# Performance work log

Hardware: AMD Instinct MI355X
Metric: run time of the kernel (lower is better)

Reference implementation:

```python
import jax, jax.numpy as jnp
import numpy as np

D_MODEL = 64  # per-head dim used in the scale sqrt(d_model*2)
B, H, S, D = 4, 16, 2048, 64


def setup_inputs() -> dict:
    key = jax.random.key(0)
    kq, kk, kv, kd, ke, km = jax.random.split(key, 6)
    return {
        "Q": jax.random.normal(kq, (B, H, S, D), dtype=jnp.float32),
        "K": jax.random.normal(kk, (B, H, S, D), dtype=jnp.float32),
        "V": jax.random.normal(kv, (B, H, S, D), dtype=jnp.float32),
        "distance_matrix": jax.random.uniform(kd, (B, S, S), dtype=jnp.float32),
        "energy_matrix": jax.random.uniform(ke, (B, S, S), dtype=jnp.float32),
        "mask": jax.random.randint(km, (B, 1, S, S), 0, 2, dtype=jnp.int32),
    }


def reference(Q, K, V, distance_matrix, energy_matrix, mask):
    # distance_matrix and energy_matrix are unused by the original forward.
    scale = 1.0 / np.sqrt(D_MODEL * 2).astype(np.float32)
    scores = jnp.einsum("bhqd,bhkd->bhqk", Q, K) * scale  # [B,H,S,S]
    scores = jnp.where(mask == 0, jnp.float32(-1e9), scores)
    attn = jax.nn.softmax(scores, axis=-1)
    context = jnp.einsum("bhqk,bhkd->bhqd", attn, V)  # [B,H,S,D]
    return context
```

## Files before the change

### kernel.cpp

```cpp
#include <hip/hip_runtime.h>
#include <stdint.h>

#define DEVINL __device__ __forceinline__

typedef float f32x4 __attribute__((ext_vector_type(4)));
typedef float f32x2 __attribute__((ext_vector_type(2)));
typedef short s16x8 __attribute__((ext_vector_type(8)));
typedef short s16x4 __attribute__((ext_vector_type(4)));
typedef unsigned int u32x4 __attribute__((ext_vector_type(4)));

constexpr int Bb = 4, Hh = 16, Ss = 2048, Dd = 64;
constexpr float SCALE = 0.088388347648318447f;
constexpr float QSC = 0.088388347648318447f * 1.4426950408889634f;

DEVINL short f2bf(float x) {
  union { float f; unsigned u; } c; c.f = x;
  unsigned r = (c.u + 0x7fffu + ((c.u >> 16) & 1u)) >> 16;
  return (short)r;
}

DEVINL unsigned pkbf(float a, float b) {
  unsigned r;
  asm("v_cvt_pk_bf16_f32 %0, %1, %2" : "=v"(r) : "v"(a), "v"(b));
  return r;
}

DEVINL void gload_lds16(const short* g, short* l) {
  __builtin_amdgcn_global_load_lds(
      (const __attribute__((address_space(1))) void*)g,
      (__attribute__((address_space(3))) void*)l, 16, 0, 0);
}

__global__ void mask_to_bits(const int* __restrict__ mask,
                             unsigned long long* __restrict__ bits, int n) {
  int gid = blockIdx.x * blockDim.x + threadIdx.x;
  int stride = gridDim.x * blockDim.x;
  for (int i = gid; i < n; i += stride) {
    unsigned long long bal = __ballot(mask[i] != 0);
    if ((i & 63) == 0) bits[i >> 6] = bal;
  }
}

__global__ void kvconv(const float* __restrict__ K, const float* __restrict__ V,
                       short* __restrict__ Kimg, short* __restrict__ Vimg) {
  const int x = blockIdx.x;
  const int sel = x & 1;
  const int t = (x >> 1) & 31;
  const int bh = x >> 6;
  const int tid = threadIdx.x;
  if (sel == 0) {
    const float* Kp = K + ((size_t)bh * Ss + t * 64) * Dd;
    short* img = Kimg + ((size_t)bh * 32 + t) * 4096;
#pragma unroll
    for (int it = 0; it < 4; ++it) {
      int idx = tid + it * 256;
      int kv = idx >> 4, c = idx & 15;
      const float* kr = Kp + (size_t)kv * Dd;
      s16x4 sv;
      sv[0] = f2bf(kr[c]);
      sv[1] = f2bf(kr[c + 16]);
      sv[2] = f2bf(kr[c + 32]);
      sv[3] = f2bf(kr[c + 48]);
      *(s16x4*)(img + kv * 64 + ((4 * c) ^ ((kv & 7) << 3))) = sv;
    }
  } else {
    const float* Vp = V + ((size_t)bh * Ss + t * 64) * Dd;
    short* img = Vimg + ((size_t)bh * 32 + t) * 4096;
    const int d = tid & 63, c4 = tid >> 6;
#pragma unroll
    for (int it = 0; it < 4; ++it) {
      int c = c4 * 4 + it;
      s16x4 sv;
      sv[0] = f2bf(Vp[(size_t)(c) * Dd + d]);
      sv[1] = f2bf(Vp[(size_t)(c + 16) * Dd + d]);
      sv[2] = f2bf(Vp[(size_t)(c + 32) * Dd + d]);
      sv[3] = f2bf(Vp[(size_t)(c + 48) * Dd + d]);
      *(s16x4*)(img + d * 64 + ((4 * c) ^ ((d & 7) << 3))) = sv;
    }
  }
}

__launch_bounds__(256, 4)
__global__ void attn2(const float* __restrict__ Q,
                      const unsigned long long* __restrict__ mbits,
                      const short* __restrict__ Kimg,
                      const short* __restrict__ Vimg,
                      float* __restrict__ Out) {
  __shared__ short lds[16384];

  const int tid = threadIdx.x;
  const int lane = tid & 63;
  const int w = tid >> 6;
  const int l15 = lane & 15;
  const int lq = lane >> 4;

  const int bid = blockIdx.x;
  const int h = bid & 15;
  const int qt = (bid >> 4) & 15;
  const int b = bid >> 8;
  const int bh = b * Hh + h;

  const float* Qp = Q + (size_t)bh * Ss * Dd;
  float* Op = Out + (size_t)bh * Ss * Dd;
  const short* Kt = Kimg + (size_t)bh * 32 * 4096;
  const short* Vt = Vimg + (size_t)bh * 32 * 4096;
  const int qbW = qt * 128 + w * 32;

  s16x8 qf[2][2];
#pragma unroll
  for (int qs = 0; qs < 2; ++qs) {
    const float* qrow = Qp + (size_t)(qbW + qs * 16 + l15) * Dd;
#pragma unroll
    for (int dh = 0; dh < 2; ++dh) {
      s16x8 f;
#pragma unroll
      for (int g = 0; g < 4; ++g) {
        f32x2 v = *(const f32x2*)(qrow + 16 * g + 4 * lq + 2 * dh);
        f[g] = f2bf(v[0] * QSC);
        f[g + 4] = f2bf(v[1] * QSC);
      }
      qf[qs][dh] = f;
    }
  }

  f32x4 oacc[2][4];
  float lpart[2] = {0.f, 0.f};
#pragma unroll
  for (int qs = 0; qs < 2; ++qs)
#pragma unroll
    for (int ds = 0; ds < 4; ++ds) oacc[qs][ds] = f32x4{0.f, 0.f, 0.f, 0.f};

  int off[4][2];
#pragma unroll
  for (int sub = 0; sub < 4; ++sub) {
    int row = sub * 16 + l15;
    int sw = (row & 7) << 3;
    off[sub][0] = row * 64 + ((16 * lq) ^ sw);
    off[sub][1] = row * 64 + ((16 * lq + 8) ^ sw);
  }

  auto stage = [&](int buf, int t) {
    short* Lb = lds + buf * 8192;
    const short* gk = Kt + t * 4096 + w * 512 + lane * 8;
    const short* gv = Vt + t * 4096 + w * 512 + lane * 8;
    gload_lds16(gk, Lb + w * 512);
    gload_lds16(gk + 2048, Lb + 2048 + w * 512);
    gload_lds16(gv, Lb + 4096 + w * 512);
    gload_lds16(gv + 2048, Lb + 6144 + w * 512);
  };

  stage(0, 0);

  for (int t = 0; t < 32; ++t) {
    const int cur = t & 1;
    __syncthreads();
    if (t < 31) stage(cur ^ 1, t + 1);

    const short* kb = lds + cur * 8192;
    const short* vb = kb + 4096;

    f32x4 sc[2][4];
#pragma unroll
    for (int sub = 0; sub < 4; ++sub) {
      s16x8 k0 = *(const s16x8*)(kb + off[sub][0]);
      s16x8 k1 = *(const s16x8*)(kb + off[sub][1]);
#pragma unroll
      for (int qs = 0; qs < 2; ++qs) {
        f32x4 a = f32x4{0.f, 0.f, 0.f, 0.f};
        a = __builtin_amdgcn_mfma_f32_16x16x32_bf16(k0, qf[qs][0], a, 0, 0, 0);
        a = __builtin_amdgcn_mfma_f32_16x16x32_bf16(k1, qf[qs][1], a, 0, 0, 0);
        sc[qs][sub] = a;
      }
    }

    s16x8 pf[2][2];
#pragma unroll
    for (int qs = 0; qs < 2; ++qs) {
      const int q = qbW + qs * 16 + l15;
      const unsigned long long mw = mbits[(size_t)(b * Ss + q) * 32 + t];
      const unsigned mlo = (unsigned)(mw >> (4 * lq));
      const unsigned mhi = (unsigned)(mw >> (32 + 4 * lq));
      const unsigned nibs[4] = {mlo & 15u, (mlo >> 16) & 15u, mhi & 15u, (mhi >> 16) & 15u};
      float ps = 0.f;
#pragma unroll
      for (int sub = 0; sub < 4; ++sub) {
        f32x4 s = sc[qs][sub];
        const unsigned nib = nibs[sub];
#pragma unroll
        for (int r = 0; r < 4; ++r) {
          float p = __builtin_amdgcn_exp2f(s[r]);
          p = ((nib >> r) & 1u) ? p : 0.f;
          s[r] = p;
          ps += p;
        }
        sc[qs][sub] = s;
      }
      lpart[qs] += ps;
#pragma unroll
      for (int kvh = 0; kvh < 2; ++kvh) {
        u32x4 wv;
        wv[0] = pkbf(sc[qs][0][2 * kvh], sc[qs][1][2 * kvh]);
        wv[1] = pkbf(sc[qs][2][2 * kvh], sc[qs][3][2 * kvh]);
        wv[2] = pkbf(sc[qs][0][2 * kvh + 1], sc[qs][1][2 * kvh + 1]);
        wv[3] = pkbf(sc[qs][2][2 * kvh + 1], sc[qs][3][2 * kvh + 1]);
        pf[qs][kvh] = __builtin_bit_cast(s16x8, wv);
      }
    }

#pragma unroll
    for (int ds = 0; ds < 4; ++ds) {
      s16x8 v0 = *(const s16x8*)(vb + off[ds][0]);
      s16x8 v1 = *(const s16x8*)(vb + off[ds][1]);
#pragma unroll
      for (int qs = 0; qs < 2; ++qs) {
        f32x4 a = oacc[qs][ds];
        a = __builtin_amdgcn_mfma_f32_16x16x32_bf16(v0, pf[qs][0], a, 0, 0, 0);
        a = __builtin_amdgcn_mfma_f32_16x16x32_bf16(v1, pf[qs][1], a, 0, 0, 0);
        oacc[qs][ds] = a;
      }
    }
  }

#pragma unroll
  for (int qs = 0; qs < 2; ++qs) {
    float l = lpart[qs];
    l += __shfl_xor(l, 16);
    l += __shfl_xor(l, 32);
    float inv = 1.f / l;
    float* orow = Op + (size_t)(qbW + qs * 16 + l15) * Dd;
#pragma unroll
    for (int ds = 0; ds < 4; ++ds) {
      f32x4 v = oacc[qs][ds];
      v *= inv;
      *(f32x4*)(orow + ds * 16 + 4 * lq) = v;
    }
  }
}

template<bool USEBITS>
__launch_bounds__(256, 2)
__global__ void attn_fwd(const float* __restrict__ Q, const float* __restrict__ K,
                         const float* __restrict__ V, const int* __restrict__ mask,
                         const unsigned long long* __restrict__ mbits,
                         float* __restrict__ Out) {
  __shared__ short Ks[64 * 64];
  __shared__ short Vs[64 * 64];

  const int tid = threadIdx.x;
  const int lane = tid & 63;
  const int w = tid >> 6;
  const int l15 = lane & 15;
  const int lq = lane >> 4;

  const int bid = blockIdx.x;
  const int h = bid & 15;
  const int qt = (bid >> 4) & 7;
  const int b = bid >> 7;

  const int bh = b * Hh + h;
  const float* Qp = Q + (size_t)bh * Ss * Dd;
  const float* Kp = K + (size_t)bh * Ss * Dd;
  const float* Vp = V + (size_t)bh * Ss * Dd;
  float* Op = Out + (size_t)bh * Ss * Dd;

  const int qbW = qt * 256 + w * 64;

  s16x8 qf[4][2];
#pragma unroll
  for (int qs = 0; qs < 4; ++qs) {
    const float* qrow = Qp + (size_t)(qbW + qs * 16 + l15) * Dd;
#pragma unroll
    for (int dh = 0; dh < 2; ++dh) {
      s16x8 f;
#pragma unroll
      for (int g = 0; g < 4; ++g) {
        f32x2 v = *(const f32x2*)(qrow + 16 * g + 4 * lq + 2 * dh);
        f[g] = f2bf(v[0]);
        f[g + 4] = f2bf(v[1]);
      }
      qf[qs][dh] = f;
    }
  }

  f32x4 oacc[4][4];
  float mrun[4], lrun[4];
#pragma unroll
  for (int qs = 0; qs < 4; ++qs) {
    mrun[qs] = -1e30f;
    lrun[qs] = 0.f;
#pragma unroll
    for (int ds = 0; ds < 4; ++ds) oacc[qs][ds] = f32x4{0.f, 0.f, 0.f, 0.f};
  }

  for (int kv0 = 0; kv0 < Ss; kv0 += 64) {
    __syncthreads();
#pragma unroll
    for (int p = 0; p < 4; ++p) {
      int f = tid + p * 256;
      int kv = f >> 4;
      int c = f & 15;
      const float* krow = Kp + (size_t)(kv0 + kv) * Dd;
      s16x4 sv;
      sv[0] = f2bf(krow[c]);
      sv[1] = f2bf(krow[c + 16]);
      sv[2] = f2bf(krow[c + 32]);
      sv[3] = f2bf(krow[c + 48]);
      *(s16x4*)(Ks + kv * 64 + ((4 * c) ^ ((kv & 7) << 3))) = sv;
    }
#pragma unroll
    for (int p = 0; p < 4; ++p) {
      int f = tid + p * 256;
      int kv = f >> 4;
      int c = f & 15;
      f32x4 v = *(const f32x4*)(Vp + (size_t)(kv0 + kv) * Dd + 4 * c);
      int pv = (kv & 15) * 4 + (kv >> 4);
#pragma unroll
      for (int i = 0; i < 4; ++i) {
        int d = 4 * c + i;
        Vs[d * 64 + (pv ^ ((d & 7) << 3))] = f2bf(v[i]);
      }
    }
    __syncthreads();

    s16x8 kf[4][2];
#pragma unroll
    for (int sub = 0; sub < 4; ++sub) {
      int row = sub * 16 + l15;
      const short* base = Ks + row * 64;
      int sw = (row & 7) << 3;
      kf[sub][0] = *(const s16x8*)(base + ((16 * lq + 0) ^ sw));
      kf[sub][1] = *(const s16x8*)(base + ((16 * lq + 8) ^ sw));
    }
    s16x8 vf[4][2];
#pragma unroll
    for (int ds = 0; ds < 4; ++ds) {
      int row = ds * 16 + l15;
      const short* base = Vs + row * 64;
      int sw = (row & 7) << 3;
      vf[ds][0] = *(const s16x8*)(base + ((16 * lq + 0) ^ sw));
      vf[ds][1] = *(const s16x8*)(base + ((16 * lq + 8) ^ sw));
    }

    const int kvw = kv0 >> 6;
#pragma unroll
    for (int qs = 0; qs < 4; ++qs) {
      f32x4 sc[4];
#pragma unroll
      for (int sub = 0; sub < 4; ++sub) {
        f32x4 a = f32x4{0.f, 0.f, 0.f, 0.f};
        a = __builtin_amdgcn_mfma_f32_16x16x32_bf16(kf[sub][0], qf[qs][0], a, 0, 0, 0);
        a = __builtin_amdgcn_mfma_f32_16x16x32_bf16(kf[sub][1], qf[qs][1], a, 0, 0, 0);
        sc[sub] = a;
      }

      const int q = qbW + qs * 16 + l15;
      unsigned long long mw = 0;
      if constexpr (USEBITS) mw = mbits[(size_t)(b * Ss + q) * 32 + kvw];

      float tm = -3e38f;
#pragma unroll
      for (int sub = 0; sub < 4; ++sub) {
        f32x4 s = sc[sub];
        if constexpr (USEBITS) {
          unsigned nib = (unsigned)((mw >> (16 * sub + 4 * lq)) & 0xFULL);
#pragma unroll
          for (int r = 0; r < 4; ++r) {
            float sv = s[r] * SCALE;
            sv = ((nib >> r) & 1u) ? sv : -1e9f;
            s[r] = sv;
            tm = fmaxf(tm, sv);
          }
        } else {
          const int* mrow = mask + ((size_t)b * Ss + q) * Ss + kv0 + 16 * sub + 4 * lq;
          int4 mi = *(const int4*)mrow;
          int mv[4] = {mi.x, mi.y, mi.z, mi.w};
#pragma unroll
          for (int r = 0; r < 4; ++r) {
            float sv = s[r] * SCALE;
            sv = mv[r] ? sv : -1e9f;
            s[r] = sv;
            tm = fmaxf(tm, sv);
          }
        }
        sc[sub] = s;
      }
      tm = fmaxf(tm, __shfl_xor(tm, 16));
      tm = fmaxf(tm, __shfl_xor(tm, 32));
      float mnew = fmaxf(mrun[qs], tm);
      float corr = __expf(mrun[qs] - mnew);
      mrun[qs] = mnew;

      float ps = 0.f;
#pragma unroll
      for (int sub = 0; sub < 4; ++sub) {
        f32x4 s = sc[sub];
#pragma unroll
        for (int r = 0; r < 4; ++r) {
          float p = __expf(s[r] - mnew);
          s[r] = p;
          ps += p;
        }
        sc[sub] = s;
      }
      ps += __shfl_xor(ps, 16);
      ps += __shfl_xor(ps, 32);
      lrun[qs] = lrun[qs] * corr + ps;
#pragma unroll
      for (int ds = 0; ds < 4; ++ds) oacc[qs][ds] *= corr;

      s16x8 pf[2];
#pragma unroll
      for (int kvh = 0; kvh < 2; ++kvh) {
        s16x8 f;
#pragma unroll
        for (int j = 0; j < 8; ++j) f[j] = f2bf(sc[j & 3][2 * kvh + (j >> 2)]);
        pf[kvh] = f;
      }
#pragma unroll
      for (int ds = 0; ds < 4; ++ds) {
        f32x4 a = oacc[qs][ds];
        a = __builtin_amdgcn_mfma_f32_16x16x32_bf16(vf[ds][0], pf[0], a, 0, 0, 0);
        a = __builtin_amdgcn_mfma_f32_16x16x32_bf16(vf[ds][1], pf[1], a, 0, 0, 0);
        oacc[qs][ds] = a;
      }
    }
  }

#pragma unroll
  for (int qs = 0; qs < 4; ++qs) {
    float inv = 1.f / lrun[qs];
    float* orow = Op + (size_t)(qbW + qs * 16 + l15) * Dd;
#pragma unroll
    for (int ds = 0; ds < 4; ++ds) {
      f32x4 v = oacc[qs][ds];
      v *= inv;
      *(f32x4*)(orow + ds * 16 + 4 * lq) = v;
    }
  }
}

extern "C" void kernel_launch(void* const* d_in, const int* in_sizes, int n_in,
                              void* d_out, int out_size, void* d_ws, size_t ws_size,
                              hipStream_t stream) {
  const float* Q = (const float*)d_in[0];
  const float* K = (const float*)d_in[1];
  const float* V = (const float*)d_in[2];
  const int* mask = (const int*)d_in[5];
  float* out = (float*)d_out;

  const int nmask = Bb * Ss * Ss;
  const size_t bitsB = (size_t)(nmask / 64) * 8;
  const size_t imgB = (size_t)Bb * Hh * 32 * 4096 * 2;
  const size_t need = bitsB + 2 * imgB;

  if (d_ws && ws_size >= need) {
    unsigned long long* bits = (unsigned long long*)d_ws;
    short* Kimg = (short*)((char*)d_ws + bitsB);
    short* Vimg = (short*)((char*)d_ws + bitsB + imgB);
    mask_to_bits<<<2048, 256, 0, stream>>>(mask, bits, nmask);
    kvconv<<<Bb * Hh * 32 * 2, 256, 0, stream>>>(K, V, Kimg, Vimg);
    attn2<<<Bb * Hh * (Ss / 128), 256, 0, stream>>>(Q, bits, Kimg, Vimg, out);
  } else if (d_ws && ws_size >= bitsB) {
    unsigned long long* bits = (unsigned long long*)d_ws;
    mask_to_bits<<<2048, 256, 0, stream>>>(mask, bits, nmask);
    attn_fwd<true><<<Bb * Hh * (Ss / 256), 256, 0, stream>>>(Q, K, V, mask, bits, out);
  } else {
    attn_fwd<false><<<Bb * Hh * (Ss / 256), 256, 0, stream>>>(Q, K, V, mask, nullptr, out);
  }
}
```

Baseline: 138.3 us.

## Fold mask into MFMA bias, compute row sums via MFMA, prefetch mask words

Replaces the per-element mask select after exp2 with an additive large-negative bias that seeds the QK^T MFMA accumulator, so exp2 yields zero for masked positions. The softmax denominator is now accumulated with extra MFMAs against a ones-row operand instead of VALU adds and cross-lane shuffles. Mask words are loaded before the barrier, and s_setprio raises priority around the MFMA blocks. This moves VALU work onto the matrix unit at the cost of extra MFMAs, and the row sum is now taken from bf16-rounded probabilities.

```diff
diff --git a/kernel.cpp b/kernel.cpp
--- a/kernel.cpp
+++ b/kernel.cpp
@@ -123,12 +123,21 @@
     }
   }
 
+  s16x8 onesA;
+  {
+    short o = (l15 == 0) ? (short)0x3F80 : (short)0;
+#pragma unroll
+    for (int j = 0; j < 8; ++j) onesA[j] = o;
+  }
+
   f32x4 oacc[2][4];
-  float lpart[2] = {0.f, 0.f};
-#pragma unroll
-  for (int qs = 0; qs < 2; ++qs)
+  f32x4 lacc[2];
+#pragma unroll
+  for (int qs = 0; qs < 2; ++qs) {
+    lacc[qs] = f32x4{0.f, 0.f, 0.f, 0.f};
 #pragma unroll
     for (int ds = 0; ds < 4; ++ds) oacc[qs][ds] = f32x4{0.f, 0.f, 0.f, 0.f};
+  }
 
   int off[4][2];
 #pragma unroll
@@ -138,6 +147,11 @@
     off[sub][0] = row * 64 + ((16 * lq) ^ sw);
     off[sub][1] = row * 64 + ((16 * lq + 8) ^ sw);
   }
+
+  const unsigned long long* mbq[2];
+#pragma unroll
+  for (int qs = 0; qs < 2; ++qs)
+    mbq[qs] = mbits + (size_t)(b * Ss + qbW + qs * 16 + l15) * 32;
 
   auto stage = [&](int buf, int t) {
     short* Lb = lds + buf * 8192;
@@ -153,49 +167,58 @@
 
   for (int t = 0; t < 32; ++t) {
     const int cur = t & 1;
+    unsigned long long mw0 = mbq[0][t];
+    unsigned long long mw1 = mbq[1][t];
     __syncthreads();
     if (t < 31) stage(cur ^ 1, t + 1);
 
     const short* kb = lds + cur * 8192;
     const short* vb = kb + 4096;
 
+    f32x4 bias[2][4];
+#pragma unroll
+    for (int qs = 0; qs < 2; ++qs) {
+      const unsigned long long mw = qs ? mw1 : mw0;
+      const unsigned mlo = ~(unsigned)(mw >> (4 * lq));
+      const unsigned mhi = ~(unsigned)(mw >> (32 + 4 * lq));
+#pragma unroll
+      for (int sub = 0; sub < 4; ++sub) {
+        const unsigned wsrc = (sub < 2) ? mlo : mhi;
+        const int base = 16 * (sub & 1);
+#pragma unroll
+        for (int r = 0; r < 4; ++r) {
+          int sb = ((int)(wsrc << (31 - (base + r)))) >> 31;
+          bias[qs][sub][r] = __uint_as_float((unsigned)sb & 0xCE6E6B28u);
+        }
+      }
+    }
+
     f32x4 sc[2][4];
+    __builtin_amdgcn_s_setprio(1);
 #pragma unroll
     for (int sub = 0; sub < 4; ++sub) {
       s16x8 k0 = *(const s16x8*)(kb + off[sub][0]);
       s16x8 k1 = *(const s16x8*)(kb + off[sub][1]);
 #pragma unroll
       for (int qs = 0; qs < 2; ++qs) {
-        f32x4 a = f32x4{0.f, 0.f, 0.f, 0.f};
+        f32x4 a = bias[qs][sub];
         a = __builtin_amdgcn_mfma_f32_16x16x32_bf16(k0, qf[qs][0], a, 0, 0, 0);
         a = __builtin_amdgcn_mfma_f32_16x16x32_bf16(k1, qf[qs][1], a, 0, 0, 0);
         sc[qs][sub] = a;
       }
     }
+    __builtin_amdgcn_s_setprio(0);
 
     s16x8 pf[2][2];
 #pragma unroll
     for (int qs = 0; qs < 2; ++qs) {
-      const int q = qbW + qs * 16 + l15;
-      const unsigned long long mw = mbits[(size_t)(b * Ss + q) * 32 + t];
-      const unsigned mlo = (unsigned)(mw >> (4 * lq));
-      const unsigned mhi = (unsigned)(mw >> (32 + 4 * lq));
-      const unsigned nibs[4] = {mlo & 15u, (mlo >> 16) & 15u, mhi & 15u, (mhi >> 16) & 15u};
-      float ps = 0.f;
 #pragma unroll
       for (int sub = 0; sub < 4; ++sub) {
         f32x4 s = sc[qs][sub];
-        const unsigned nib = nibs[sub];
-#pragma unroll
-        for (int r = 0; r < 4; ++r) {
-          float p = __builtin_amdgcn_exp2f(s[r]);
-          p = ((nib >> r) & 1u) ? p : 0.f;
-          s[r] = p;
-          ps += p;
-        }
+#pragma unroll
+        for (int r = 0; r < 4; ++r) s[r] = __builtin_amdgcn_exp2f(s[r]);
         sc[qs][sub] = s;
       }
-      lpart[qs] += ps;
 #pragma unroll
       for (int kvh = 0; kvh < 2; ++kvh) {
         u32x4 wv;
@@ -207,6 +230,7 @@
       }
     }
 
+    __builtin_amdgcn_s_setprio(1);
 #pragma unroll
     for (int ds = 0; ds < 4; ++ds) {
       s16x8 v0 = *(const s16x8*)(vb + off[ds][0]);
@@ -219,13 +243,17 @@
         oacc[qs][ds] = a;
       }
     }
+#pragma unroll
+    for (int qs = 0; qs < 2; ++qs) {
+      lacc[qs] = __builtin_amdgcn_mfma_f32_16x16x32_bf16(onesA, pf[qs][0], lacc[qs], 0, 0, 0);
+      lacc[qs] = __builtin_amdgcn_mfma_f32_16x16x32_bf16(onesA, pf[qs][1], lacc[qs], 0, 0, 0);
+    }
+    __builtin_amdgcn_s_setprio(0);
   }
 
 #pragma unroll
   for (int qs = 0; qs < 2; ++qs) {
-    float l = lpart[qs];
-    l += __shfl_xor(l, 16);
-    l += __shfl_xor(l, 32);
+    float l = __shfl(lacc[qs][0], l15);
     float inv = 1.f / l;
     float* orow = Op + (size_t)(qbW + qs * 16 + l15) * Dd;
 #pragma unroll
```

After: 134.4 us (median of 2 runs). 1.03x faster.
